# Performance work log

Measured on AMD Instinct MI355X. Metric: run time of the kernel, lower is better.

The kernel has to match this reference:

```python
import jax, jax.numpy as jnp
import numpy as np
import math

DIM = 4096
N_HEADS = 32
N_KV_HEADS = 8
HEAD_DIM = DIM // N_HEADS  # 128
ROPE_THETA = 500000.0
SEQ_LEN = 1
START_IDX = 8191
CACHE_LEN = START_IDX + SEQ_LEN  # 8192


def _rope(x, cos, sin):
    # x: [s, h, d]; cos/sin: [s, d//2]. Strided (even/odd) RoPE as in source.
    xe = x[:, :, 0::2]
    xo = x[:, :, 1::2]
    c = cos[:, None, :]
    s = sin[:, None, :]
    re = xe * c - xo * s
    ro = xe * s + xo * c
    # interleave back: [..., d//2, 2] -> [..., d]
    return jnp.stack([re, ro], axis=-1).reshape(x.shape)


def setup_inputs() -> dict:
    key = jax.random.key(0)
    ks = jax.random.split(key, 7)
    sc = 0.02
    return {
        "x": jax.random.normal(ks[0], (SEQ_LEN, DIM), jnp.float32),
        "wq": jax.random.normal(ks[1], (DIM, DIM), jnp.float32) * sc,
        "wk": jax.random.normal(ks[2], (N_KV_HEADS * HEAD_DIM, DIM), jnp.float32) * sc,
        "wv": jax.random.normal(ks[3], (N_KV_HEADS * HEAD_DIM, DIM), jnp.float32) * sc,
        "wo": jax.random.normal(ks[4], (DIM, DIM), jnp.float32) * sc,
        "k_cache": jax.random.normal(ks[5], (CACHE_LEN, N_KV_HEADS, HEAD_DIM), jnp.float32),
        "v_cache": jax.random.normal(ks[6], (CACHE_LEN, N_KV_HEADS, HEAD_DIM), jnp.float32),
        "start_idx": START_IDX,
    }


def reference(x, wq, wk, wv, wo, k_cache, v_cache, start_idx):
    seq_len = x.shape[0]
    # QKV projections (matmul with w.T as in source)
    Q = (x @ wq.T).reshape(seq_len, N_HEADS, HEAD_DIM)
    K = (x @ wk.T).reshape(seq_len, N_KV_HEADS, HEAD_DIM)
    V = (x @ wv.T).reshape(seq_len, N_KV_HEADS, HEAD_DIM)

    # RoPE frequencies for positions [start_idx, start_idx+seq_len)
    inv_freq = 1.0 / (ROPE_THETA ** (jnp.arange(0, HEAD_DIM, 2, dtype=jnp.float32) / HEAD_DIM))
    t = jnp.arange(start_idx, start_idx + seq_len, dtype=jnp.float32)
    freqs = t[:, None] * inv_freq[None, :]  # [s, d/2]
    cos, sin = jnp.cos(freqs), jnp.sin(freqs)

    Q = _rope(Q, cos, sin)
    K = _rope(K, cos, sin)

    # KV-cache append (start_idx is a static Python int)
    kc = jax.lax.dynamic_update_slice(k_cache, K, (start_idx, 0, 0))
    vc = jax.lax.dynamic_update_slice(v_cache, V, (start_idx, 0, 0))
    total = start_idx + seq_len
    keys = kc[:total]    # [T, kvh, d]
    values = vc[:total]

    rep = N_HEADS // N_KV_HEADS
    Kr = jnp.repeat(keys, rep, axis=1)    # [T, h, d] (repeat_interleave)
    Vr = jnp.repeat(values, rep, axis=1)

    scale = 1.0 / math.sqrt(HEAD_DIM)
    scores = jnp.einsum('qhd,khd->hqk', Q, Kr) * scale  # [h, s, T]

    if seq_len > 1:
        q_pos = jnp.arange(seq_len)[:, None] + start_idx
        k_pos = jnp.arange(total)[None, :]
        mask = jnp.where(k_pos > q_pos, jnp.float32(-jnp.inf), 0.0)
        scores = scores + mask[None, :, :]

    probs = jax.nn.softmax(scores.astype(jnp.float32), axis=-1).astype(Q.dtype)
    out = jnp.einsum('hqk,khd->qhd', probs, Vr).reshape(seq_len, N_HEADS * HEAD_DIM)
    return out @ wo.T
```

## Files before the change

kernel.cpp:

```cpp
#include <hip/hip_runtime.h>
#include <math.h>

#define DIM 4096
#define HD 128
#define NH 32
#define NKV 8
#define CACHE_LEN 8192
#define NCHUNK 128
#define CHUNK 64
#define SCALE 0.08838834764831845f

__global__ __launch_bounds__(64) void rope_table_kernel(
    const int* __restrict__ start_idx_p, float* __restrict__ tab )
{
    const int p = threadIdx.x;
    const float te   = (float)pow(500000.0, (double)p * (1.0/64.0));
    const float invf = 1.0f / te;
    const float freq = (float)(*start_idx_p) * invf;
    const double ang = (double)freq;
    tab[p]      = (float)cos(ang);
    tab[64 + p] = (float)sin(ang);
}

__global__ __launch_bounds__(256) void qkv_rope_kernel(
    const float* __restrict__ x, const float* __restrict__ wq,
    const float* __restrict__ wk, const float* __restrict__ wv,
    float* __restrict__ k_cache, float* __restrict__ v_cache,
    const int* __restrict__ start_idx_p, const float* __restrict__ tab,
    float* __restrict__ q_out)
{
    const int wave = threadIdx.x >> 6;
    const int lane = threadIdx.x & 63;
    const int r0   = blockIdx.x * 2;
    const int rrow = r0 + (wave >> 1);
    const int sub  = wave & 1;

    const float* w;
    if (rrow < DIM)                w = wq + (size_t)rrow * DIM;
    else if (rrow < DIM + NKV*HD)  w = wk + (size_t)(rrow - DIM) * DIM;
    else                           w = wv + (size_t)(rrow - DIM - NKV*HD) * DIM;

    const float4* w4 = (const float4*)w + sub*512;
    const float4* x4 = (const float4*)x + sub*512;
    float acc = 0.f;
#pragma unroll
    for (int it = 0; it < 8; ++it) {
        float4 a = w4[it*64 + lane];
        float4 b = x4[it*64 + lane];
        acc = fmaf(a.x, b.x, acc); acc = fmaf(a.y, b.y, acc);
        acc = fmaf(a.z, b.z, acc); acc = fmaf(a.w, b.w, acc);
    }
#pragma unroll
    for (int off = 32; off > 0; off >>= 1) acc += __shfl_down(acc, off);

    __shared__ float dots[4];
    if (lane == 0) dots[wave] = acc;
    __syncthreads();

    if (threadIdx.x == 0) {
        const float de = dots[0] + dots[1];
        const float dd = dots[2] + dots[3];
        const int sidx = *start_idx_p;
        if (r0 < DIM + NKV*HD) {
            const int local = (r0 < DIM) ? r0 : r0 - DIM;
            const int p = (local & (HD-1)) >> 1;
            const float c = tab[p], s = tab[64 + p];
            const float re = de * c - dd * s;
            const float ro = de * s + dd * c;
            if (r0 < DIM) {
                q_out[r0] = re; q_out[r0+1] = ro;
            } else {
                const size_t base = (size_t)sidx * (NKV*HD) + (size_t)(r0 - DIM);
                k_cache[base] = re; k_cache[base+1] = ro;
            }
        } else {
            const size_t base = (size_t)sidx * (NKV*HD) + (size_t)(r0 - DIM - NKV*HD);
            v_cache[base] = de; v_cache[base+1] = dd;
        }
    }
}

__global__ __launch_bounds__(256) void attn_partial_kernel(
    const float* __restrict__ q, const float* __restrict__ k_cache,
    const float* __restrict__ v_cache,
    float* __restrict__ part_acc,
    float* __restrict__ part_l)
{
    const int kv    = blockIdx.x >> 7;
    const int chunk = blockIdx.x & (NCHUNK-1);
    const int wave  = threadIdx.x >> 6;
    const int lane  = threadIdx.x & 63;
    const int g  = lane >> 4;
    const int gl = lane & 15;

    float4 q0[4], q1[4];
#pragma unroll
    for (int hh = 0; hh < 4; ++hh) {
        const float* qb = q + (size_t)(kv*4 + hh) * HD;
        float4 a = *(const float4*)(qb + gl*4);
        float4 b = *(const float4*)(qb + 64 + gl*4);
        a.x *= SCALE; a.y *= SCALE; a.z *= SCALE; a.w *= SCALE;
        b.x *= SCALE; b.y *= SCALE; b.z *= SCALE; b.w *= SCALE;
        q0[hh] = a; q1[hh] = b;
    }

    float acc0[4][4] = {{0}}, acc1[4][4] = {{0}};
    float lsum[4] = {0.f, 0.f, 0.f, 0.f};

    const int pbase = chunk*CHUNK + wave*16 + g*4;
#pragma unroll
    for (int it = 0; it < 4; it += 2) {
        const int posA = pbase + it, posB = pbase + it + 1;
        const float* kA = k_cache + ((size_t)posA*NKV + kv) * HD;
        const float* kB = k_cache + ((size_t)posB*NKV + kv) * HD;
        const float* vA = v_cache + ((size_t)posA*NKV + kv) * HD;
        const float* vB = v_cache + ((size_t)posB*NKV + kv) * HD;
        float4 k0A = *(const float4*)(kA + gl*4);
        float4 k1A = *(const float4*)(kA + 64 + gl*4);
        float4 k0B = *(const float4*)(kB + gl*4);
        float4 k1B = *(const float4*)(kB + 64 + gl*4);
        float4 v0A = *(const float4*)(vA + gl*4);
        float4 v1A = *(const float4*)(vA + 64 + gl*4);
        float4 v0B = *(const float4*)(vB + gl*4);
        float4 v1B = *(const float4*)(vB + 64 + gl*4);

        float sA[4], sB[4];
#pragma unroll
        for (int hh = 0; hh < 4; ++hh) {
            float t;
            t  = q0[hh].x*k0A.x + q0[hh].y*k0A.y + q0[hh].z*k0A.z + q0[hh].w*k0A.w;
            t += q1[hh].x*k1A.x + q1[hh].y*k1A.y + q1[hh].z*k1A.z + q1[hh].w*k1A.w;
            sA[hh] = t;
            t  = q0[hh].x*k0B.x + q0[hh].y*k0B.y + q0[hh].z*k0B.z + q0[hh].w*k0B.w;
            t += q1[hh].x*k1B.x + q1[hh].y*k1B.y + q1[hh].z*k1B.z + q1[hh].w*k1B.w;
            sB[hh] = t;
        }
#pragma unroll
        for (int off = 1; off < 16; off <<= 1) {
#pragma unroll
            for (int hh = 0; hh < 4; ++hh) {
                sA[hh] += __shfl_xor(sA[hh], off);
                sB[hh] += __shfl_xor(sB[hh], off);
            }
        }
#pragma unroll
        for (int hh = 0; hh < 4; ++hh) {
            const float pA = expf(sA[hh]);
            const float pB = expf(sB[hh]);
            lsum[hh] += pA + pB;
            acc0[hh][0] = fmaf(pA, v0A.x, fmaf(pB, v0B.x, acc0[hh][0]));
            acc0[hh][1] = fmaf(pA, v0A.y, fmaf(pB, v0B.y, acc0[hh][1]));
            acc0[hh][2] = fmaf(pA, v0A.z, fmaf(pB, v0B.z, acc0[hh][2]));
            acc0[hh][3] = fmaf(pA, v0A.w, fmaf(pB, v0B.w, acc0[hh][3]));
            acc1[hh][0] = fmaf(pA, v1A.x, fmaf(pB, v1B.x, acc1[hh][0]));
            acc1[hh][1] = fmaf(pA, v1A.y, fmaf(pB, v1B.y, acc1[hh][1]));
            acc1[hh][2] = fmaf(pA, v1A.z, fmaf(pB, v1B.z, acc1[hh][2]));
            acc1[hh][3] = fmaf(pA, v1A.w, fmaf(pB, v1B.w, acc1[hh][3]));
        }
    }

#pragma unroll
    for (int off = 16; off < 64; off <<= 1) {
#pragma unroll
        for (int hh = 0; hh < 4; ++hh) {
            lsum[hh] += __shfl_xor(lsum[hh], off);
#pragma unroll
            for (int j = 0; j < 4; ++j) {
                acc0[hh][j] += __shfl_xor(acc0[hh][j], off);
                acc1[hh][j] += __shfl_xor(acc1[hh][j], off);
            }
        }
    }

    __shared__ float red[4][4*HD];
    __shared__ float lred[4][4];
    if (lane < 16) {
#pragma unroll
        for (int hh = 0; hh < 4; ++hh) {
            *(float4*)&red[wave][hh*HD + gl*4] =
                make_float4(acc0[hh][0], acc0[hh][1], acc0[hh][2], acc0[hh][3]);
            *(float4*)&red[wave][hh*HD + 64 + gl*4] =
                make_float4(acc1[hh][0], acc1[hh][1], acc1[hh][2], acc1[hh][3]);
        }
        if (gl == 0) {
            lred[wave][0] = lsum[0]; lred[wave][1] = lsum[1];
            lred[wave][2] = lsum[2]; lred[wave][3] = lsum[3];
        }
    }
    __syncthreads();

    float* outp = part_acc + (size_t)blockIdx.x * (4*HD);
#pragma unroll
    for (int k = 0; k < 2; ++k) {
        const int idx = (int)threadIdx.x + k*256;
        outp[idx] = red[0][idx] + red[1][idx] + red[2][idx] + red[3][idx];
    }
    if (threadIdx.x < 4) {
        part_l[(size_t)blockIdx.x*4 + threadIdx.x] =
            lred[0][threadIdx.x] + lred[1][threadIdx.x] +
            lred[2][threadIdx.x] + lred[3][threadIdx.x];
    }
}

__global__ __launch_bounds__(128) void attn_combine_kernel(
    const float* __restrict__ part_acc, const float* __restrict__ part_l,
    float* __restrict__ attn_out)
{
    const int h  = blockIdx.x;
    const int kv = h >> 2, hh = h & 3;
    const int d  = threadIdx.x;
    float acc = 0.f, l = 0.f;
    for (int c = 0; c < NCHUNK; ++c) {
        const int pid = kv*NCHUNK + c;
        acc += part_acc[(size_t)pid*(4*HD) + hh*HD + d];
        l   += part_l[pid*4 + hh];
    }
    attn_out[h*HD + d] = acc / l;
}

__global__ __launch_bounds__(256) void out_proj_kernel(
    const float* __restrict__ attn, const float* __restrict__ wo,
    float* __restrict__ out)
{
    const int row = blockIdx.x;
    const float4* w4 = (const float4*)(wo + (size_t)row * DIM);
    const float4* a4 = (const float4*)attn;
    float acc = 0.f;
#pragma unroll
    for (int it = 0; it < 4; ++it) {
        float4 a = w4[it*256 + threadIdx.x];
        float4 b = a4[it*256 + threadIdx.x];
        acc = fmaf(a.x, b.x, acc); acc = fmaf(a.y, b.y, acc);
        acc = fmaf(a.z, b.z, acc); acc = fmaf(a.w, b.w, acc);
    }
#pragma unroll
    for (int off = 32; off > 0; off >>= 1) acc += __shfl_down(acc, off);
    __shared__ float dots[4];
    if ((threadIdx.x & 63) == 0) dots[threadIdx.x >> 6] = acc;
    __syncthreads();
    if (threadIdx.x == 0) out[row] = dots[0] + dots[1] + dots[2] + dots[3];
}

extern "C" void kernel_launch(void* const* d_in, const int* in_sizes, int n_in,
                              void* d_out, int out_size, void* d_ws, size_t ws_size,
                              hipStream_t stream)
{
    const float* x  = (const float*)d_in[0];
    const float* wq = (const float*)d_in[1];
    const float* wk = (const float*)d_in[2];
    const float* wv = (const float*)d_in[3];
    const float* wo = (const float*)d_in[4];
    float* k_cache  = (float*)d_in[5];
    float* v_cache  = (float*)d_in[6];
    const int* sidx = (const int*)d_in[7];
    float* out = (float*)d_out;

    float* ws       = (float*)d_ws;
    float* q        = ws;
    float* part_acc = ws + 4096;
    float* part_l   = part_acc + 1024*512;
    float* attn     = part_l + 4096;
    float* tab      = attn + 4096;

    hipLaunchKernelGGL(rope_table_kernel, dim3(1), dim3(64), 0, stream, sidx, tab);
    hipLaunchKernelGGL(qkv_rope_kernel, dim3((DIM + NKV*HD*2)/2), dim3(256), 0, stream,
                       x, wq, wk, wv, k_cache, v_cache, sidx, tab, q);
    hipLaunchKernelGGL(attn_partial_kernel, dim3(NKV*NCHUNK), dim3(256), 0, stream,
                       q, k_cache, v_cache, part_acc, part_l);
    hipLaunchKernelGGL(attn_combine_kernel, dim3(NH), dim3(HD), 0, stream,
                       part_acc, part_l, attn);
    hipLaunchKernelGGL(out_proj_kernel, dim3(DIM), dim3(256), 0, stream,
                       attn, wo, out);
}
```

Before: 246.7 us.

## Fuse all stages into one cooperative persistent kernel with grid syncs

Replaces five separate kernel launches with a single cooperative kernel of 1024 blocks that runs rope table, QKV projection, attention partials, combine and output projection, separated by grid.sync. The goal is to remove per-launch overhead and inter-kernel gaps. It also regroups the combine stage into 128 small tasks of 32 dims each, computes each output-projection row with a single wave, and moves the V loads after the score reduction. The cost is four grid-wide barriers, which are expensive on a large GPU, and less parallelism in the QKV and out-projection stages. If the cooperative launch fails, the code falls back to separate kernels.

```diff
diff --git a/kernel.cpp b/kernel.cpp
--- a/kernel.cpp
+++ b/kernel.cpp
@@ -1,19 +1,22 @@
 #include <hip/hip_runtime.h>
+#include <hip/hip_cooperative_groups.h>
 #include <math.h>
+
+namespace cg = cooperative_groups;
 
 #define DIM 4096
 #define HD 128
 #define NH 32
 #define NKV 8
-#define CACHE_LEN 8192
 #define NCHUNK 128
 #define CHUNK 64
+#define GRID 1024
 #define SCALE 0.08838834764831845f
 
-__global__ __launch_bounds__(64) void rope_table_kernel(
-    const int* __restrict__ start_idx_p, float* __restrict__ tab )
-{
-    const int p = threadIdx.x;
+
+__device__ __forceinline__ void rope_table_body(int p, const int* start_idx_p,
+                                                float* tab)
+{
     const float te   = (float)pow(500000.0, (double)p * (1.0/64.0));
     const float invf = 1.0f / te;
     const float freq = (float)(*start_idx_p) * invf;
@@ -22,24 +25,21 @@
     tab[64 + p] = (float)sin(ang);
 }
 
-__global__ __launch_bounds__(256) void qkv_rope_kernel(
+__device__ __forceinline__ void qkv_pair_body(
+    int r0, int wave, int lane, int tid, float dots[4],
     const float* __restrict__ x, const float* __restrict__ wq,
     const float* __restrict__ wk, const float* __restrict__ wv,
     float* __restrict__ k_cache, float* __restrict__ v_cache,
     const int* __restrict__ start_idx_p, const float* __restrict__ tab,
-    float* __restrict__ q_out)
-{
-    const int wave = threadIdx.x >> 6;
-    const int lane = threadIdx.x & 63;
-    const int r0   = blockIdx.x * 2;
-    const int rrow = r0 + (wave >> 1);
+    float* __restrict__ q_buf)
+{
+    const int rsub = wave >> 1;
     const int sub  = wave & 1;
-
+    const int rrow = r0 + rsub;
     const float* w;
     if (rrow < DIM)                w = wq + (size_t)rrow * DIM;
     else if (rrow < DIM + NKV*HD)  w = wk + (size_t)(rrow - DIM) * DIM;
     else                           w = wv + (size_t)(rrow - DIM - NKV*HD) * DIM;
-
     const float4* w4 = (const float4*)w + sub*512;
     const float4* x4 = (const float4*)x + sub*512;
     float acc = 0.f;
@@ -47,17 +47,14 @@
     for (int it = 0; it < 8; ++it) {
         float4 a = w4[it*64 + lane];
         float4 b = x4[it*64 + lane];
-        acc = fmaf(a.x, b.x, acc); acc = fmaf(a.y, b.y, acc);
-        acc = fmaf(a.z, b.z, acc); acc = fmaf(a.w, b.w, acc);
+        acc = fmaf(a.x,b.x,acc); acc = fmaf(a.y,b.y,acc);
+        acc = fmaf(a.z,b.z,acc); acc = fmaf(a.w,b.w,acc);
     }
 #pragma unroll
     for (int off = 32; off > 0; off >>= 1) acc += __shfl_down(acc, off);
-
-    __shared__ float dots[4];
     if (lane == 0) dots[wave] = acc;
     __syncthreads();
-
-    if (threadIdx.x == 0) {
+    if (tid == 0) {
         const float de = dots[0] + dots[1];
         const float dd = dots[2] + dots[3];
         const int sidx = *start_idx_p;
@@ -65,38 +62,37 @@
             const int local = (r0 < DIM) ? r0 : r0 - DIM;
             const int p = (local & (HD-1)) >> 1;
             const float c = tab[p], s = tab[64 + p];
-            const float re = de * c - dd * s;
-            const float ro = de * s + dd * c;
-            if (r0 < DIM) {
-                q_out[r0] = re; q_out[r0+1] = ro;
-            } else {
-                const size_t base = (size_t)sidx * (NKV*HD) + (size_t)(r0 - DIM);
+            const float re = de*c - dd*s;
+            const float ro = de*s + dd*c;
+            if (r0 < DIM) { q_buf[r0] = re; q_buf[r0+1] = ro; }
+            else {
+                const size_t base = (size_t)sidx*(NKV*HD) + (size_t)(r0 - DIM);
                 k_cache[base] = re; k_cache[base+1] = ro;
             }
         } else {
-            const size_t base = (size_t)sidx * (NKV*HD) + (size_t)(r0 - DIM - NKV*HD);
+            const size_t base = (size_t)sidx*(NKV*HD) + (size_t)(r0 - DIM - NKV*HD);
             v_cache[base] = de; v_cache[base+1] = dd;
         }
     }
-}
-
-__global__ __launch_bounds__(256) void attn_partial_kernel(
-    const float* __restrict__ q, const float* __restrict__ k_cache,
+    __syncthreads();
+}
+
+__device__ __forceinline__ void attn_partial_body(
+    int taskid, int wave, int lane, int tid,
+    float red[4][4*HD], float lred[4][4],
+    const float* __restrict__ q_buf, const float* __restrict__ k_cache,
     const float* __restrict__ v_cache,
-    float* __restrict__ part_acc,
-    float* __restrict__ part_l)
-{
-    const int kv    = blockIdx.x >> 7;
-    const int chunk = blockIdx.x & (NCHUNK-1);
-    const int wave  = threadIdx.x >> 6;
-    const int lane  = threadIdx.x & 63;
+    float* __restrict__ part_acc, float* __restrict__ part_l)
+{
+    const int kv    = taskid >> 7;
+    const int chunk = taskid & (NCHUNK-1);
     const int g  = lane >> 4;
     const int gl = lane & 15;
 
     float4 q0[4], q1[4];
 #pragma unroll
     for (int hh = 0; hh < 4; ++hh) {
-        const float* qb = q + (size_t)(kv*4 + hh) * HD;
+        const float* qb = q_buf + (size_t)(kv*4 + hh) * HD;
         float4 a = *(const float4*)(qb + gl*4);
         float4 b = *(const float4*)(qb + 64 + gl*4);
         a.x *= SCALE; a.y *= SCALE; a.z *= SCALE; a.w *= SCALE;
@@ -113,36 +109,35 @@
         const int posA = pbase + it, posB = pbase + it + 1;
         const float* kA = k_cache + ((size_t)posA*NKV + kv) * HD;
         const float* kB = k_cache + ((size_t)posB*NKV + kv) * HD;
-        const float* vA = v_cache + ((size_t)posA*NKV + kv) * HD;
-        const float* vB = v_cache + ((size_t)posB*NKV + kv) * HD;
         float4 k0A = *(const float4*)(kA + gl*4);
         float4 k1A = *(const float4*)(kA + 64 + gl*4);
         float4 k0B = *(const float4*)(kB + gl*4);
         float4 k1B = *(const float4*)(kB + 64 + gl*4);
+        float sA[4], sB[4];
+#pragma unroll
+        for (int hh = 0; hh < 4; ++hh) {
+            float t1;
+            t1  = q0[hh].x*k0A.x + q0[hh].y*k0A.y + q0[hh].z*k0A.z + q0[hh].w*k0A.w;
+            t1 += q1[hh].x*k1A.x + q1[hh].y*k1A.y + q1[hh].z*k1A.z + q1[hh].w*k1A.w;
+            sA[hh] = t1;
+            t1  = q0[hh].x*k0B.x + q0[hh].y*k0B.y + q0[hh].z*k0B.z + q0[hh].w*k0B.w;
+            t1 += q1[hh].x*k1B.x + q1[hh].y*k1B.y + q1[hh].z*k1B.z + q1[hh].w*k1B.w;
+            sB[hh] = t1;
+        }
+#pragma unroll
+        for (int off = 1; off < 16; off <<= 1) {
+#pragma unroll
+            for (int hh = 0; hh < 4; ++hh) {
+                sA[hh] += __shfl_xor(sA[hh], off);
+                sB[hh] += __shfl_xor(sB[hh], off);
+            }
+        }
+        const float* vA = v_cache + ((size_t)posA*NKV + kv) * HD;
+        const float* vB = v_cache + ((size_t)posB*NKV + kv) * HD;
         float4 v0A = *(const float4*)(vA + gl*4);
         float4 v1A = *(const float4*)(vA + 64 + gl*4);
         float4 v0B = *(const float4*)(vB + gl*4);
         float4 v1B = *(const float4*)(vB + 64 + gl*4);
-
-        float sA[4], sB[4];
-#pragma unroll
-        for (int hh = 0; hh < 4; ++hh) {
-            float t;
-            t  = q0[hh].x*k0A.x + q0[hh].y*k0A.y + q0[hh].z*k0A.z + q0[hh].w*k0A.w;
-            t += q1[hh].x*k1A.x + q1[hh].y*k1A.y + q1[hh].z*k1A.z + q1[hh].w*k1A.w;
-            sA[hh] = t;
-            t  = q0[hh].x*k0B.x + q0[hh].y*k0B.y + q0[hh].z*k0B.z + q0[hh].w*k0B.w;
-            t += q1[hh].x*k1B.x + q1[hh].y*k1B.y + q1[hh].z*k1B.z + q1[hh].w*k1B.w;
-            sB[hh] = t;
-        }
-#pragma unroll
-        for (int off = 1; off < 16; off <<= 1) {
-#pragma unroll
-            for (int hh = 0; hh < 4; ++hh) {
-                sA[hh] += __shfl_xor(sA[hh], off);
-                sB[hh] += __shfl_xor(sB[hh], off);
-            }
-        }
 #pragma unroll
         for (int hh = 0; hh < 4; ++hh) {
             const float pA = expf(sA[hh]);
@@ -172,8 +167,6 @@
         }
     }
 
-    __shared__ float red[4][4*HD];
-    __shared__ float lred[4][4];
     if (lane < 16) {
 #pragma unroll
         for (int hh = 0; hh < 4; ++hh) {
@@ -189,56 +182,139 @@
     }
     __syncthreads();
 
-    float* outp = part_acc + (size_t)blockIdx.x * (4*HD);
+    float* outp = part_acc + (size_t)taskid * (4*HD);
 #pragma unroll
     for (int k = 0; k < 2; ++k) {
-        const int idx = (int)threadIdx.x + k*256;
+        const int idx = tid + k*256;
         outp[idx] = red[0][idx] + red[1][idx] + red[2][idx] + red[3][idx];
     }
-    if (threadIdx.x < 4) {
-        part_l[(size_t)blockIdx.x*4 + threadIdx.x] =
-            lred[0][threadIdx.x] + lred[1][threadIdx.x] +
-            lred[2][threadIdx.x] + lred[3][threadIdx.x];
-    }
-}
-
-__global__ __launch_bounds__(128) void attn_combine_kernel(
+    if (tid < 4) {
+        part_l[(size_t)taskid*4 + tid] =
+            lred[0][tid] + lred[1][tid] + lred[2][tid] + lred[3][tid];
+    }
+}
+
+__device__ __forceinline__ void combine_body(
+    int taskid, int tid,
     const float* __restrict__ part_acc, const float* __restrict__ part_l,
-    float* __restrict__ attn_out)
-{
-    const int h  = blockIdx.x;
-    const int kv = h >> 2, hh = h & 3;
-    const int d  = threadIdx.x;
-    float acc = 0.f, l = 0.f;
-    for (int c = 0; c < NCHUNK; ++c) {
-        const int pid = kv*NCHUNK + c;
-        acc += part_acc[(size_t)pid*(4*HD) + hh*HD + d];
-        l   += part_l[pid*4 + hh];
-    }
-    attn_out[h*HD + d] = acc / l;
+    float* __restrict__ attn)
+{
+    const int h  = taskid >> 2;
+    const int dq = taskid & 3;
+    if (tid < 32) {
+        const int d   = dq*32 + tid;
+        const int kvh = h >> 2, hh = h & 3;
+        float acc = 0.f, l = 0.f;
+        for (int c = 0; c < NCHUNK; ++c) {
+            const int pid = kvh*NCHUNK + c;
+            acc += part_acc[(size_t)pid*(4*HD) + hh*HD + d];
+            l   += part_l[pid*4 + hh];
+        }
+        attn[h*HD + d] = acc / l;
+    }
+}
+
+__device__ __forceinline__ void out_proj_body(
+    int row, int lane, const float* __restrict__ attn,
+    const float* __restrict__ wo, float* __restrict__ out)
+{
+    const float4* w4 = (const float4*)(wo + (size_t)row * DIM);
+    const float4* a4 = (const float4*)attn;
+    float acc = 0.f;
+#pragma unroll
+    for (int it = 0; it < 16; ++it) {
+        float4 a = w4[it*64 + lane];
+        float4 b = a4[it*64 + lane];
+        acc = fmaf(a.x,b.x,acc); acc = fmaf(a.y,b.y,acc);
+        acc = fmaf(a.z,b.z,acc); acc = fmaf(a.w,b.w,acc);
+    }
+#pragma unroll
+    for (int off = 32; off > 0; off >>= 1) acc += __shfl_down(acc, off);
+    if (lane == 0) out[row] = acc;
+}
+
+__global__ __launch_bounds__(256, 4) void mha_mega(
+    const float* __restrict__ x, const float* __restrict__ wq,
+    const float* __restrict__ wk, const float* __restrict__ wv,
+    const float* __restrict__ wo,
+    float* __restrict__ k_cache, float* __restrict__ v_cache,
+    const int* __restrict__ start_idx_p,
+    float* __restrict__ q_buf, float* __restrict__ part_acc,
+    float* __restrict__ part_l, float* __restrict__ attn,
+    float* __restrict__ tab, float* __restrict__ out)
+{
+    cg::grid_group grid = cg::this_grid();
+    const int bid  = blockIdx.x;
+    const int tid  = threadIdx.x;
+    const int wave = tid >> 6;
+    const int lane = tid & 63;
+
+    __shared__ float dots[4];
+    __shared__ float red[4][4*HD];
+    __shared__ float lred[4][4];
+
+    if (bid == 0 && tid < 64) rope_table_body(tid, start_idx_p, tab);
+    grid.sync();
+
+    for (int t = 0; t < 3; ++t)
+        qkv_pair_body((bid + t*GRID) * 2, wave, lane, tid, dots,
+                      x, wq, wk, wv, k_cache, v_cache, start_idx_p, tab, q_buf);
+    grid.sync();
+
+    attn_partial_body(bid, wave, lane, tid, red, lred,
+                      q_buf, k_cache, v_cache, part_acc, part_l);
+    grid.sync();
+
+    if (bid < 128) combine_body(bid, tid, part_acc, part_l, attn);
+    grid.sync();
+
+    out_proj_body(bid*4 + wave, lane, attn, wo, out);
+}
+
+__global__ __launch_bounds__(64) void rope_table_kernel(
+    const int* __restrict__ start_idx_p, float* __restrict__ tab)
+{
+    rope_table_body(threadIdx.x, start_idx_p, tab);
+}
+
+__global__ __launch_bounds__(256) void qkv_rope_kernel(
+    const float* __restrict__ x, const float* __restrict__ wq,
+    const float* __restrict__ wk, const float* __restrict__ wv,
+    float* __restrict__ k_cache, float* __restrict__ v_cache,
+    const int* __restrict__ start_idx_p, const float* __restrict__ tab,
+    float* __restrict__ q_buf)
+{
+    __shared__ float dots[4];
+    qkv_pair_body(blockIdx.x * 2, threadIdx.x >> 6, threadIdx.x & 63,
+                  threadIdx.x, dots, x, wq, wk, wv, k_cache, v_cache,
+                  start_idx_p, tab, q_buf);
+}
+
+__global__ __launch_bounds__(256) void attn_partial_kernel(
+    const float* __restrict__ q_buf, const float* __restrict__ k_cache,
+    const float* __restrict__ v_cache,
+    float* __restrict__ part_acc, float* __restrict__ part_l)
+{
+    __shared__ float red[4][4*HD];
+    __shared__ float lred[4][4];
+    attn_partial_body(blockIdx.x, threadIdx.x >> 6, threadIdx.x & 63,
+                      threadIdx.x, red, lred, q_buf, k_cache, v_cache,
+                      part_acc, part_l);
+}
+
+__global__ __launch_bounds__(64) void attn_combine_kernel(
+    const float* __restrict__ part_acc, const float* __restrict__ part_l,
+    float* __restrict__ attn)
+{
+    combine_body(blockIdx.x, threadIdx.x, part_acc, part_l, attn);
 }
 
 __global__ __launch_bounds__(256) void out_proj_kernel(
     const float* __restrict__ attn, const float* __restrict__ wo,
     float* __restrict__ out)
 {
-    const int row = blockIdx.x;
-    const float4* w4 = (const float4*)(wo + (size_t)row * DIM);
-    const float4* a4 = (const float4*)attn;
-    float acc = 0.f;
-#pragma unroll
-    for (int it = 0; it < 4; ++it) {
-        float4 a = w4[it*256 + threadIdx.x];
-        float4 b = a4[it*256 + threadIdx.x];
-        acc = fmaf(a.x, b.x, acc); acc = fmaf(a.y, b.y, acc);
-        acc = fmaf(a.z, b.z, acc); acc = fmaf(a.w, b.w, acc);
-    }
-#pragma unroll
-    for (int off = 32; off > 0; off >>= 1) acc += __shfl_down(acc, off);
-    __shared__ float dots[4];
-    if ((threadIdx.x & 63) == 0) dots[threadIdx.x >> 6] = acc;
-    __syncthreads();
-    if (threadIdx.x == 0) out[row] = dots[0] + dots[1] + dots[2] + dots[3];
+    out_proj_body(blockIdx.x*4 + (threadIdx.x >> 6), threadIdx.x & 63,
+                  attn, wo, out);
 }
 
 extern "C" void kernel_launch(void* const* d_in, const int* in_sizes, int n_in,
@@ -256,19 +332,29 @@
     float* out = (float*)d_out;
 
     float* ws       = (float*)d_ws;
-    float* q        = ws;
+    float* q_buf    = ws;
     float* part_acc = ws + 4096;
     float* part_l   = part_acc + 1024*512;
-    float* attn     = part_l + 4096;
-    float* tab      = attn + 4096;
-
-    hipLaunchKernelGGL(rope_table_kernel, dim3(1), dim3(64), 0, stream, sidx, tab);
-    hipLaunchKernelGGL(qkv_rope_kernel, dim3((DIM + NKV*HD*2)/2), dim3(256), 0, stream,
-                       x, wq, wk, wv, k_cache, v_cache, sidx, tab, q);
-    hipLaunchKernelGGL(attn_partial_kernel, dim3(NKV*NCHUNK), dim3(256), 0, stream,
-                       q, k_cache, v_cache, part_acc, part_l);
-    hipLaunchKernelGGL(attn_combine_kernel, dim3(NH), dim3(HD), 0, stream,
-                       part_acc, part_l, attn);
-    hipLaunchKernelGGL(out_proj_kernel, dim3(DIM), dim3(256), 0, stream,
-                       attn, wo, out);
-}
+    float* attn_buf = part_l + 4096;
+    float* tab      = attn_buf + 4096;
+
+    void* args[] = { (void*)&x, (void*)&wq, (void*)&wk, (void*)&wv, (void*)&wo,
+                     (void*)&k_cache, (void*)&v_cache, (void*)&sidx,
+                     (void*)&q_buf, (void*)&part_acc, (void*)&part_l,
+                     (void*)&attn_buf, (void*)&tab, (void*)&out };
+    hipError_t err = hipLaunchCooperativeKernel((void*)mha_mega, dim3(GRID),
+                                                dim3(256), args, 0, stream);
+    if (err != hipSuccess) {
+        hipLaunchKernelGGL(rope_table_kernel, dim3(1), dim3(64), 0, stream,
+                           sidx, tab);
+        hipLaunchKernelGGL(qkv_rope_kernel, dim3((DIM + NKV*HD*2)/2), dim3(256),
+                           0, stream, x, wq, wk, wv, k_cache, v_cache, sidx,
+                           tab, q_buf);
+        hipLaunchKernelGGL(attn_partial_kernel, dim3(NKV*NCHUNK), dim3(256),
+                           0, stream, q_buf, k_cache, v_cache, part_acc, part_l);
+        hipLaunchKernelGGL(attn_combine_kernel, dim3(NH*4), dim3(64), 0, stream,
+                           part_acc, part_l, attn_buf);
+        hipLaunchKernelGGL(out_proj_kernel, dim3(DIM/4), dim3(256), 0, stream,
+                           attn_buf, wo, out);
+    }
+}
```

Measured after the change: 636.7 us. +158.1%, slower.
